# Kernel optimization log

Measured on AMD Instinct MI355X. Metric: run time of the kernel, lower is better.

## Reference

```python
import jax, jax.numpy as jnp
import numpy as np

B, C_IN, C_OUT, H, W = 4, 256, 256, 64, 64
K, STRIDE, PAD, DIL = 3, 1, 1, 1
KK = K * K


def setup_inputs() -> dict:
    key = jax.random.key(0)
    k1, k2, k3, k4 = jax.random.split(key, 4)
    x = jax.random.normal(k1, (B, C_IN, H, W), jnp.float32)
    # offset/mask conv weight (no bias), scaled small so offsets are modest
    w_mod = jax.random.normal(k2, (3 * KK, C_IN, K, K), jnp.float32) * 0.01
    # deform conv weight (xavier-ish scale) + bias
    w_def = jax.random.normal(k3, (C_OUT, C_IN, K, K), jnp.float32) * (1.0 / np.sqrt(C_IN * KK))
    b_def = jax.random.normal(k4, (C_OUT,), jnp.float32) * 0.01
    return {"x": x, "w_mod": w_mod, "w_def": w_def, "b_def": b_def}


def _conv_nchw(x, w, stride, pad):
    return jax.lax.conv_general_dilated(
        x, w, (stride, stride), [(pad, pad), (pad, pad)],
        dimension_numbers=("NCHW", "OIHW", "NCHW"))


def _bilinear_sample(x, py, px):
    # x: [B,C,H,W]; py/px: [B,KK,Ho,Wo] absolute sample coords (zero-pad outside)
    Bn, Cc, Hh, Ww = x.shape
    y0 = jnp.floor(py)
    x0 = jnp.floor(px)
    fy = py - y0
    fx = px - x0
    y0i = y0.astype(jnp.int32)
    x0i = x0.astype(jnp.int32)
    xf = x.reshape(Bn, Cc, Hh * Ww)

    def corner(yi, xi, wgt):
        valid = (yi >= 0) & (yi < Hh) & (xi >= 0) & (xi < Ww)
        yc = jnp.clip(yi, 0, Hh - 1)
        xc = jnp.clip(xi, 0, Ww - 1)
        idx = yc * Ww + xc                      # [B,KK,Ho,Wo]
        g = jax.vmap(lambda f, i: f[:, i])(xf, idx)  # [B,C,KK,Ho,Wo]
        return g * (wgt * valid)[:, None]

    return (corner(y0i, x0i, (1 - fy) * (1 - fx))
            + corner(y0i, x0i + 1, (1 - fy) * fx)
            + corner(y0i + 1, x0i, fy * (1 - fx))
            + corner(y0i + 1, x0i + 1, fy * fx))


def reference(x, w_mod, w_def, b_def):
    # offset/mask head
    mod = _conv_nchw(x, w_mod, STRIDE, PAD)          # [B, 3*KK, Ho, Wo]
    o1, o2, mask = mod[:, :KK], mod[:, KK:2 * KK], mod[:, 2 * KK:]
    offset = jnp.concatenate([o1, o2], axis=1)        # [B, 2*KK, Ho, Wo]
    # torchvision DeformConv2d: offset channels are interleaved (y, x) pairs
    dy = offset[:, 0::2]
    dx = offset[:, 1::2]
    mask = jax.nn.sigmoid(mask)                       # [B, KK, Ho, Wo]

    Ho, Wo = mod.shape[2], mod.shape[3]
    ky, kx = jnp.meshgrid(jnp.arange(K), jnp.arange(K), indexing="ij")
    ky = ky.reshape(-1).astype(jnp.float32)
    kx = kx.reshape(-1).astype(jnp.float32)
    base_y = (jnp.arange(Ho, dtype=jnp.float32) * STRIDE - PAD)[None, :, None] + (ky * DIL)[:, None, None]  # [KK,Ho,1]
    base_x = (jnp.arange(Wo, dtype=jnp.float32) * STRIDE - PAD)[None, None, :] + (kx * DIL)[:, None, None]  # [KK,1,Wo]
    py = dy + base_y[None]                            # [B,KK,Ho,Wo]
    px = dx + base_x[None]

    sampled = _bilinear_sample(x, py, px) * mask[:, None]  # [B,C,KK,Ho,Wo]
    out = jnp.einsum("bckhw,ock->bohw", sampled, w_def.reshape(C_OUT, C_IN, KK))
    return out + b_def[None, :, None, None]
```

## Files before the change

### kernel.cpp

```cpp
#include <hip/hip_runtime.h>

typedef unsigned short u16;
typedef unsigned int u32;
typedef short bf16x8 __attribute__((ext_vector_type(8)));
typedef float f32x4 __attribute__((ext_vector_type(4)));

#define CIN 256
#define COUT 256

__device__ __forceinline__ u16 f2b(float f) {
  u32 u = __float_as_uint(f);
  u += 0x7fffu + ((u >> 16) & 1u);
  return (u16)(u >> 16);
}
__device__ __forceinline__ u32 packbf(float lo, float hi) {
  return (u32)f2b(lo) | ((u32)f2b(hi) << 16);
}
__device__ __forceinline__ u32 bil2(u32 u00, u32 u01, u32 u10, u32 u11, float4 wt) {
  float s0 = __uint_as_float(u00 << 16) * wt.x;
  s0 = fmaf(__uint_as_float(u01 << 16), wt.y, s0);
  s0 = fmaf(__uint_as_float(u10 << 16), wt.z, s0);
  s0 = fmaf(__uint_as_float(u11 << 16), wt.w, s0);
  float s1 = __uint_as_float(u00 & 0xffff0000u) * wt.x;
  s1 = fmaf(__uint_as_float(u01 & 0xffff0000u), wt.y, s1);
  s1 = fmaf(__uint_as_float(u10 & 0xffff0000u), wt.z, s1);
  s1 = fmaf(__uint_as_float(u11 & 0xffff0000u), wt.w, s1);
  return packbf(s0, s1);
}
__device__ __forceinline__ void bar() {
  asm volatile("s_waitcnt lgkmcnt(0)\n\ts_barrier" ::: "memory");
}

__global__ __launch_bounds__(256) void k_prep(
    const float* __restrict__ x, const float* __restrict__ w_mod,
    const float* __restrict__ w_def,
    u16* __restrict__ xT, u16* __restrict__ Wm2, u16* __restrict__ W2) {
  __shared__ __align__(16) char SB[9216];
  int t = threadIdx.x, g = blockIdx.x;
  if (g < 1024) {
    u16 (*T)[72] = (u16(*)[72])SB;
    int b = g >> 8, ct = (g >> 6) & 3, pt = g & 63;
    int c0 = ct << 6, pos0 = pt << 6;
    {
      int cl = t >> 2, pb = (t & 3) << 4;
      const float* p = x + (((b << 8) + c0 + cl) << 12) + pos0 + pb;
#pragma unroll
      for (int i = 0; i < 4; ++i) {
        float4 v = *(const float4*)(p + i * 4);
        int pp = pb + i * 4;
        T[pp][cl] = f2b(v.x); T[pp + 1][cl] = f2b(v.y);
        T[pp + 2][cl] = f2b(v.z); T[pp + 3][cl] = f2b(v.w);
      }
    }
    __syncthreads();
    {
      int pl = t >> 2, q = t & 3;
      u16* dst = xT + (((b << 12) + pos0 + pl) << 8) + c0 + (q << 4);
      *(uint4*)dst = *(const uint4*)&T[pl][q << 4];
      *(uint4*)(dst + 8) = *(const uint4*)&T[pl][(q << 4) + 8];
    }
  } else {
    float* L = (float*)SB;
    int gg = g - 1024;
    if (gg < 256) {
      const float* src = w_def + gg * 2304;
      for (int j = t; j < 2304; j += 256) L[j] = src[j];
      __syncthreads();
      u16* dst = W2 + gg * 2304;
      for (int j = t; j < 2304; j += 256) {
        int kk = j >> 8, c = j & 255;
        dst[j] = f2b(L[c * 9 + kk]);
      }
    } else {
      int cm = gg - 256;
      if (cm < 27) {
        const float* src = w_mod + cm * 2304;
        for (int j = t; j < 2304; j += 256) L[j] = src[j];
      }
      __syncthreads();
      u16* dst = Wm2 + cm * 2304;
      for (int j = t; j < 2304; j += 256) {
        int kk = j >> 8, c = j & 255;
        dst[j] = (cm < 27) ? f2b(L[c * 9 + kk]) : (u16)0;
      }
    }
  }
}

__global__ __launch_bounds__(512) void k_fused(
    const u16* __restrict__ xT, const u16* __restrict__ Wm2,
    const u16* __restrict__ W2, const float* __restrict__ b_def,
    float* __restrict__ out) {
  __shared__ __align__(16) char LB[53760];
  __shared__ __align__(16) int2 Ci[576];
  __shared__ __align__(16) float4 Cw[576];
  u16 (*As1)[2][64][72] = (u16 (*)[2][64][72])LB;
  float (*mods2)[32][66] = (float (*)[32][66])(LB + 36864);
  u16 (*As2)[64][72] = (u16 (*)[64][72])LB;

  int t = threadIdx.x;
  int l = t & 63;
  int w = t >> 6;
  int h = t >> 8;
  int wl = w & 3;
  int tg = t & 255;
  int px = tg >> 2, q = tg & 3;
  int g = blockIdx.x;
  int b = (g & 7) >> 1, y = ((g >> 3) << 1) + (g & 1);
  const u16* xTb = xT + (b << 20);
  int ml = l & 15, kq = l >> 4;

  {
    f32x4 zero = {0.f, 0.f, 0.f, 0.f};
    f32x4 acc0 = zero, acc1 = zero;
    uint4 VA0, VA1, VB0, VB1;
    uint4 S0, S1, S2, S3, T0, T1, T2, T3;

#define MC_ISSUE_A(i, V0, V1)                                                \
  { int ch_ = h * 18 + (i); int kk_ = ch_ >> 2, c0_ = (ch_ & 3) << 6;        \
    int ky_ = kk_ / 3, kx_ = kk_ - 3 * ky_;                                  \
    int ys_ = y + ky_ - 1, xs_ = px + kx_ - 1;                               \
    V0 = make_uint4(0, 0, 0, 0); V1 = V0;                                    \
    if (ys_ >= 0 && ys_ < 64 && xs_ >= 0 && xs_ < 64) {                      \
      const u16* p_ = xTb + (((ys_ << 6) + xs_) << 8) + c0_ + (q << 4);      \
      V0 = *(const uint4*)p_; V1 = *(const uint4*)(p_ + 8);                  \
    } }

#define MC_ISSUE_B(i, R0, R1, R2, R3)                                        \
  { int ch_ = h * 18 + (i); int kk_ = ch_ >> 2, c0_ = (ch_ & 3) << 6;        \
    const u16* pw_ = Wm2 + (kk_ << 8) + c0_ + (kq << 3);                     \
    R0 = *(const uint4*)(pw_ + ml * 2304);                                   \
    R1 = *(const uint4*)(pw_ + (16 + ml) * 2304);                            \
    R2 = *(const uint4*)(pw_ + ml * 2304 + 32);                              \
    R3 = *(const uint4*)(pw_ + (16 + ml) * 2304 + 32); }

#define MC_WRITE(buf, V0, V1)                                                \
  { *(uint4*)&As1[h][buf][px][q << 4] = V0;                                  \
    *(uint4*)&As1[h][buf][px][(q << 4) + 8] = V1; }

#define MC_MFMA(buf, R0, R1, R2, R3)                                         \
  { bf16x8 a0_ = *(const bf16x8*)&As1[h][buf][wl * 16 + ml][kq << 3];        \
    acc0 = __builtin_amdgcn_mfma_f32_16x16x32_bf16(a0_, *(const bf16x8*)&R0, acc0, 0,0,0); \
    acc1 = __builtin_amdgcn_mfma_f32_16x16x32_bf16(a0_, *(const bf16x8*)&R1, acc1, 0,0,0); \
    bf16x8 a1_ = *(const bf16x8*)&As1[h][buf][wl * 16 + ml][32 + (kq << 3)]; \
    acc0 = __builtin_amdgcn_mfma_f32_16x16x32_bf16(a1_, *(const bf16x8*)&R2, acc0, 0,0,0); \
    acc1 = __builtin_amdgcn_mfma_f32_16x16x32_bf16(a1_, *(const bf16x8*)&R3, acc1, 0,0,0); }

    MC_ISSUE_A(0, VA0, VA1)
    MC_ISSUE_A(1, VB0, VB1)
    MC_ISSUE_B(0, S0, S1, S2, S3)
#pragma unroll 1
    for (int i2 = 0; i2 < 18; i2 += 2) {
      MC_WRITE(0, VA0, VA1)
      bar();
      if (i2 + 2 < 18) MC_ISSUE_A(i2 + 2, VA0, VA1)
      MC_ISSUE_B(i2 + 1, T0, T1, T2, T3)
      MC_MFMA(0, S0, S1, S2, S3)
      MC_WRITE(1, VB0, VB1)
      bar();
      if (i2 + 3 < 18) MC_ISSUE_A(i2 + 3, VB0, VB1)
      if (i2 + 2 < 18) MC_ISSUE_B(i2 + 2, S0, S1, S2, S3)
      MC_MFMA(1, T0, T1, T2, T3)
    }
#pragma unroll
    for (int r = 0; r < 4; ++r) {
      mods2[h][ml][wl * 16 + kq * 4 + r]      = acc0[r];
      mods2[h][16 + ml][wl * 16 + kq * 4 + r] = acc1[r];
    }
    __syncthreads();
    for (int i2 = t; i2 < 576; i2 += 512) {
      int kk = i2 >> 6, pxx_i = i2 & 63;
      float dy = mods2[0][2 * kk][pxx_i] + mods2[1][2 * kk][pxx_i];
      float dx = mods2[0][2 * kk + 1][pxx_i] + mods2[1][2 * kk + 1][pxx_i];
      float mv = mods2[0][18 + kk][pxx_i] + mods2[1][18 + kk][pxx_i];
      float msk = 1.f / (1.f + __expf(-mv));
      int ky = kk / 3, kx = kk - 3 * ky;
      float py  = dy + (float)(y + ky - 1);
      float pxx = dx + (float)(pxx_i + kx - 1);
      float y0f = floorf(py), x0f = floorf(pxx);
      float fy = py - y0f, fx = pxx - x0f;
      int y0 = (int)y0f, x0 = (int)x0f;
      float vy0 = (y0 >= 0 && y0 < 64) ? msk : 0.f;
      float vy1 = (y0 + 1 >= 0 && y0 + 1 < 64) ? msk : 0.f;
      float w00 = (1.f - fy) * (1.f - fx) * vy0;
      float w01 = (1.f - fy) * fx * vy0;
      float w10 = fy * (1.f - fx) * vy1;
      float w11 = fy * fx * vy1;
      int xb2 = min(max(x0, 0), 62);
      float wA0 = (xb2 == x0) ? w00 : ((xb2 == x0 + 1) ? w01 : 0.f);
      float wB0 = (xb2 + 1 == x0) ? w00 : ((xb2 + 1 == x0 + 1) ? w01 : 0.f);
      float wA1 = (xb2 == x0) ? w10 : ((xb2 == x0 + 1) ? w11 : 0.f);
      float wB1 = (xb2 + 1 == x0) ? w10 : ((xb2 + 1 == x0 + 1) ? w11 : 0.f);
      int ib0 = min(max(y0, 0), 63) * 64 + xb2;
      int ib1 = min(max(y0 + 1, 0), 63) * 64 + xb2;
      Ci[i2] = make_int2(ib0, ib1);
      Cw[i2] = make_float4(wA0, wB0, wA1, wB1);
    }
#undef MC_ISSUE_A
#undef MC_ISSUE_B
#undef MC_WRITE
#undef MC_MFMA
  }
  __syncthreads();

  {
    int gm = t >> 3, go = t & 7;
    int nrow0 = w * 32 + ml, nrow1 = nrow0 + 16;

    f32x4 zero = {0.f, 0.f, 0.f, 0.f};
    f32x4 acc[4][2];
#pragma unroll
    for (int i = 0; i < 4; ++i) { acc[i][0] = zero; acc[i][1] = zero; }

    uint4 A00, A01, A02, A03; float4 wt0;
    uint4 A10, A11, A12, A13; float4 wt1;
    uint4 RA0, RA1, RA2, RA3;
    uint4 RB0, RB1, RB2, RB3;

#define ISSUE_A(chunk, a0, a1, a2, a3, wt)                                   \
  { int kk_ = (chunk) >> 2, c0_ = ((chunk) & 3) << 6;                        \
    int cI_ = (kk_ << 6) + gm;                                               \
    int2 ib_ = Ci[cI_];                                                      \
    wt = Cw[cI_];                                                            \
    const u16* p0_ = xTb + (ib_.x << 8) + c0_ + (go << 3);                   \
    const u16* p1_ = xTb + (ib_.y << 8) + c0_ + (go << 3);                   \
    a0 = *(const uint4*)p0_;  a1 = *(const uint4*)(p0_ + 256);               \
    a2 = *(const uint4*)p1_;  a3 = *(const uint4*)(p1_ + 256); }

#define ISSUE_B(chunk, R0, R1, R2, R3)                                       \
  { int kk_ = (chunk) >> 2, c0_ = ((chunk) & 3) << 6;                        \
    const u16* pw_ = W2 + (kk_ << 8) + c0_ + (kq << 3);                      \
    R0 = *(const uint4*)(pw_ + nrow0 * 2304);                                \
    R1 = *(const uint4*)(pw_ + nrow1 * 2304);                                \
    R2 = *(const uint4*)(pw_ + nrow0 * 2304 + 32);                           \
    R3 = *(const uint4*)(pw_ + nrow1 * 2304 + 32); }

#define UNPACK(CUR, a0, a1, a2, a3, wt)                                      \
  { u32 q0_ = bil2(a0.x, a1.x, a2.x, a3.x, wt);                              \
    u32 q1_ = bil2(a0.y, a1.y, a2.y, a3.y, wt);                              \
    u32 q2_ = bil2(a0.z, a1.z, a2.z, a3.z, wt);                              \
    u32 q3_ = bil2(a0.w, a1.w, a2.w, a3.w, wt);                              \
    *(uint4*)&As2[CUR][gm][go << 3] = make_uint4(q0_, q1_, q2_, q3_); }

#define DOMFMA(CUR, R0, R1, R2, R3)                                          \
  { bf16x8 a0_ = *(const bf16x8*)&As2[CUR][ml][kq << 3];                     \
    bf16x8 a1_ = *(const bf16x8*)&As2[CUR][16 + ml][kq << 3];                \
    bf16x8 a2_ = *(const bf16x8*)&As2[CUR][32 + ml][kq << 3];                \
    bf16x8 a3_ = *(const bf16x8*)&As2[CUR][48 + ml][kq << 3];                \
    bf16x8 b0_ = *(const bf16x8*)&R0;                                        \
    bf16x8 b1_ = *(const bf16x8*)&R1;                                        \
    acc[0][0] = __builtin_amdgcn_mfma_f32_16x16x32_bf16(a0_, b0_, acc[0][0], 0,0,0); \
    acc[1][0] = __builtin_amdgcn_mfma_f32_16x16x32_bf16(a1_, b0_, acc[1][0], 0,0,0); \
    acc[2][0] = __builtin_amdgcn_mfma_f32_16x16x32_bf16(a2_, b0_, acc[2][0], 0,0,0); \
    acc[3][0] = __builtin_amdgcn_mfma_f32_16x16x32_bf16(a3_, b0_, acc[3][0], 0,0,0); \
    acc[0][1] = __builtin_amdgcn_mfma_f32_16x16x32_bf16(a0_, b1_, acc[0][1], 0,0,0); \
    acc[1][1] = __builtin_amdgcn_mfma_f32_16x16x32_bf16(a1_, b1_, acc[1][1], 0,0,0); \
    acc[2][1] = __builtin_amdgcn_mfma_f32_16x16x32_bf16(a2_, b1_, acc[2][1], 0,0,0); \
    acc[3][1] = __builtin_amdgcn_mfma_f32_16x16x32_bf16(a3_, b1_, acc[3][1], 0,0,0); \
    a0_ = *(const bf16x8*)&As2[CUR][ml][32 + (kq << 3)];                     \
    a1_ = *(const bf16x8*)&As2[CUR][16 + ml][32 + (kq << 3)];                \
    a2_ = *(const bf16x8*)&As2[CUR][32 + ml][32 + (kq << 3)];                \
    a3_ = *(const bf16x8*)&As2[CUR][48 + ml][32 + (kq << 3)];                \
    b0_ = *(const bf16x8*)&R2;                                               \
    b1_ = *(const bf16x8*)&R3;                                               \
    acc[0][0] = __builtin_amdgcn_mfma_f32_16x16x32_bf16(a0_, b0_, acc[0][0], 0,0,0); \
    acc[1][0] = __builtin_amdgcn_mfma_f32_16x16x32_bf16(a1_, b0_, acc[1][0], 0,0,0); \
    acc[2][0] = __builtin_amdgcn_mfma_f32_16x16x32_bf16(a2_, b0_, acc[2][0], 0,0,0); \
    acc[3][0] = __builtin_amdgcn_mfma_f32_16x16x32_bf16(a3_, b0_, acc[3][0], 0,0,0); \
    acc[0][1] = __builtin_amdgcn_mfma_f32_16x16x32_bf16(a0_, b1_, acc[0][1], 0,0,0); \
    acc[1][1] = __builtin_amdgcn_mfma_f32_16x16x32_bf16(a1_, b1_, acc[1][1], 0,0,0); \
    acc[2][1] = __builtin_amdgcn_mfma_f32_16x16x32_bf16(a2_, b1_, acc[2][1], 0,0,0); \
    acc[3][1] = __builtin_amdgcn_mfma_f32_16x16x32_bf16(a3_, b1_, acc[3][1], 0,0,0); }

    ISSUE_A(0, A00, A01, A02, A03, wt0)
    ISSUE_A(1, A10, A11, A12, A13, wt1)
    ISSUE_B(0, RA0, RA1, RA2, RA3)
#pragma unroll 1
    for (int c2 = 0; c2 < 36; c2 += 2) {
      UNPACK(0, A00, A01, A02, A03, wt0)
      bar();
      if (c2 + 2 < 36) ISSUE_A(c2 + 2, A00, A01, A02, A03, wt0)
      ISSUE_B(c2 + 1, RB0, RB1, RB2, RB3)
      DOMFMA(0, RA0, RA1, RA2, RA3)
      UNPACK(1, A10, A11, A12, A13, wt1)
      bar();
      if (c2 + 3 < 36) ISSUE_A(c2 + 3, A10, A11, A12, A13, wt1)
      if (c2 + 2 < 36) ISSUE_B(c2 + 2, RA0, RA1, RA2, RA3)
      DOMFMA(1, RB0, RB1, RB2, RB3)
    }

#pragma unroll
    for (int nt = 0; nt < 2; ++nt) {
      int n = w * 32 + nt * 16 + ml;
      float bias = b_def[n];
      float* op = out + (((b << 8) + n) << 12) + (y << 6);
#pragma unroll
      for (int mt = 0; mt < 4; ++mt) {
        float4 v;
        v.x = acc[mt][nt][0] + bias;
        v.y = acc[mt][nt][1] + bias;
        v.z = acc[mt][nt][2] + bias;
        v.w = acc[mt][nt][3] + bias;
        *(float4*)(op + mt * 16 + kq * 4) = v;
      }
    }
#undef ISSUE_A
#undef ISSUE_B
#undef UNPACK
#undef DOMFMA
  }
}

extern "C" void kernel_launch(void* const* d_in, const int* in_sizes, int n_in,
                              void* d_out, int out_size, void* d_ws, size_t ws_size,
                              hipStream_t stream) {
  const float* x     = (const float*)d_in[0];
  const float* w_mod = (const float*)d_in[1];
  const float* w_def = (const float*)d_in[2];
  const float* b_def = (const float*)d_in[3];
  float* out = (float*)d_out;
  char* ws = (char*)d_ws;
  u16* xT  = (u16*)(ws);
  u16* W2  = (u16*)(ws + 8388608);
  u16* Wm2 = (u16*)(ws + 8388608 + 1179648);

  hipLaunchKernelGGL(k_prep, dim3(1312), dim3(256), 0, stream, x, w_mod, w_def, xT, Wm2, W2);
  hipLaunchKernelGGL(k_fused, dim3(256), dim3(512), 0, stream, xT, Wm2, W2, b_def, out);
}
```

Before: 155.2 us.

## Process four K-chunks per barrier pair with deeper weight-register prefetch

Restructures the main MFMA loop so each iteration unpacks two gathered A chunks into shared memory, synchronises once, then runs MFMAs on both. Weight-fragment prefetch moves from two register sets to four (SA/SB/TA/TB), keeping B loads two chunks ahead. The aim is to halve the number of workgroup barriers per K chunk and give global loads more time to land before use. In exchange it raises register pressure, which may lower occupancy. It also needs four shared-memory A buffers, and that declaration does not appear in the change.

```diff
diff --git a/kernel.cpp b/kernel.cpp
--- a/kernel.cpp
+++ b/kernel.cpp
@@ -214,8 +214,10 @@
 
     uint4 A00, A01, A02, A03; float4 wt0;
     uint4 A10, A11, A12, A13; float4 wt1;
-    uint4 RA0, RA1, RA2, RA3;
-    uint4 RB0, RB1, RB2, RB3;
+    uint4 SA0, SA1, SA2, SA3;
+    uint4 SB0, SB1, SB2, SB3;
+    uint4 TA0, TA1, TA2, TA3;
+    uint4 TB0, TB1, TB2, TB3;
 
 #define ISSUE_A(chunk, a0, a1, a2, a3, wt)                                   \
   { int kk_ = (chunk) >> 2, c0_ = ((chunk) & 3) << 6;                        \
@@ -274,19 +276,31 @@
 
     ISSUE_A(0, A00, A01, A02, A03, wt0)
     ISSUE_A(1, A10, A11, A12, A13, wt1)
-    ISSUE_B(0, RA0, RA1, RA2, RA3)
+    ISSUE_B(0, SA0, SA1, SA2, SA3)
+    ISSUE_B(1, SB0, SB1, SB2, SB3)
 #pragma unroll 1
-    for (int c2 = 0; c2 < 36; c2 += 2) {
+    for (int p2 = 0; p2 < 9; ++p2) {
+      int c4 = p2 << 2;
       UNPACK(0, A00, A01, A02, A03, wt0)
-      bar();
-      if (c2 + 2 < 36) ISSUE_A(c2 + 2, A00, A01, A02, A03, wt0)
-      ISSUE_B(c2 + 1, RB0, RB1, RB2, RB3)
-      DOMFMA(0, RA0, RA1, RA2, RA3)
       UNPACK(1, A10, A11, A12, A13, wt1)
       bar();
-      if (c2 + 3 < 36) ISSUE_A(c2 + 3, A10, A11, A12, A13, wt1)
-      if (c2 + 2 < 36) ISSUE_B(c2 + 2, RA0, RA1, RA2, RA3)
-      DOMFMA(1, RB0, RB1, RB2, RB3)
+      ISSUE_A(c4 + 2, A00, A01, A02, A03, wt0)
+      ISSUE_A(c4 + 3, A10, A11, A12, A13, wt1)
+      ISSUE_B(c4 + 2, TA0, TA1, TA2, TA3)
+      ISSUE_B(c4 + 3, TB0, TB1, TB2, TB3)
+      DOMFMA(0, SA0, SA1, SA2, SA3)
+      DOMFMA(1, SB0, SB1, SB2, SB3)
+      UNPACK(2, A00, A01, A02, A03, wt0)
+      UNPACK(3, A10, A11, A12, A13, wt1)
+      bar();
+      if (p2 < 8) {
+        ISSUE_A(c4 + 4, A00, A01, A02, A03, wt0)
+        ISSUE_A(c4 + 5, A10, A11, A12, A13, wt1)
+        ISSUE_B(c4 + 4, SA0, SA1, SA2, SA3)
+        ISSUE_B(c4 + 5, SB0, SB1, SB2, SB3)
+      }
+      DOMFMA(2, TA0, TA1, TA2, TA3)
+      DOMFMA(3, TB0, TB1, TB2, TB3)
     }
 
 #pragma unroll
```

New measurement: 156.0 us. No clear change (+0.5%).

## Double block to 1024 threads and split deform GEMM across channel-chunk halves

Applied to the files above, without the earlier changes.

The fused kernel now launches 1024 threads per block. The offset/mask conv still runs on the first 512 threads while the others only match its barriers. The bilinear coefficient setup now uses one thread per entry. In the main deform GEMM each wave owns 16 output channels instead of 32, and the two block halves handle interleaved input-channel chunks through four LDS buffers. The aim is more resident waves per CU to hide gather and weight-load latency with a smaller per-thread accumulator, at the cost of tighter register budgets, idle threads in phase one and more barrier participants.

```diff
diff --git a/kernel.cpp b/kernel.cpp
--- a/kernel.cpp
+++ b/kernel.cpp
@@ -87,7 +87,7 @@
   }
 }
 
-__global__ __launch_bounds__(512) void k_fused(
+__global__ __launch_bounds__(1024) void k_fused(
     const u16* __restrict__ xT, const u16* __restrict__ Wm2,
     const u16* __restrict__ W2, const float* __restrict__ b_def,
     float* __restrict__ out) {
@@ -101,16 +101,16 @@
   int t = threadIdx.x;
   int l = t & 63;
   int w = t >> 6;
-  int h = t >> 8;
-  int wl = w & 3;
-  int tg = t & 255;
-  int px = tg >> 2, q = tg & 3;
   int g = blockIdx.x;
   int b = (g & 7) >> 1, y = ((g >> 3) << 1) + (g & 1);
   const u16* xTb = xT + (b << 20);
   int ml = l & 15, kq = l >> 4;
 
-  {
+  if (t < 512) {
+    int h = t >> 8;
+    int wl = (t >> 6) & 3;
+    int tg = t & 255;
+    int px = tg >> 2, q = tg & 3;
     f32x4 zero = {0.f, 0.f, 0.f, 0.f};
     f32x4 acc0 = zero, acc1 = zero;
     uint4 VA0, VA1, VB0, VB1;
@@ -167,55 +167,62 @@
       mods2[h][ml][wl * 16 + kq * 4 + r]      = acc0[r];
       mods2[h][16 + ml][wl * 16 + kq * 4 + r] = acc1[r];
     }
-    __syncthreads();
-    for (int i2 = t; i2 < 576; i2 += 512) {
-      int kk = i2 >> 6, pxx_i = i2 & 63;
-      float dy = mods2[0][2 * kk][pxx_i] + mods2[1][2 * kk][pxx_i];
-      float dx = mods2[0][2 * kk + 1][pxx_i] + mods2[1][2 * kk + 1][pxx_i];
-      float mv = mods2[0][18 + kk][pxx_i] + mods2[1][18 + kk][pxx_i];
-      float msk = 1.f / (1.f + __expf(-mv));
-      int ky = kk / 3, kx = kk - 3 * ky;
-      float py  = dy + (float)(y + ky - 1);
-      float pxx = dx + (float)(pxx_i + kx - 1);
-      float y0f = floorf(py), x0f = floorf(pxx);
-      float fy = py - y0f, fx = pxx - x0f;
-      int y0 = (int)y0f, x0 = (int)x0f;
-      float vy0 = (y0 >= 0 && y0 < 64) ? msk : 0.f;
-      float vy1 = (y0 + 1 >= 0 && y0 + 1 < 64) ? msk : 0.f;
-      float w00 = (1.f - fy) * (1.f - fx) * vy0;
-      float w01 = (1.f - fy) * fx * vy0;
-      float w10 = fy * (1.f - fx) * vy1;
-      float w11 = fy * fx * vy1;
-      int xb2 = min(max(x0, 0), 62);
-      float wA0 = (xb2 == x0) ? w00 : ((xb2 == x0 + 1) ? w01 : 0.f);
-      float wB0 = (xb2 + 1 == x0) ? w00 : ((xb2 + 1 == x0 + 1) ? w01 : 0.f);
-      float wA1 = (xb2 == x0) ? w10 : ((xb2 == x0 + 1) ? w11 : 0.f);
-      float wB1 = (xb2 + 1 == x0) ? w10 : ((xb2 + 1 == x0 + 1) ? w11 : 0.f);
-      int ib0 = min(max(y0, 0), 63) * 64 + xb2;
-      int ib1 = min(max(y0 + 1, 0), 63) * 64 + xb2;
-      Ci[i2] = make_int2(ib0, ib1);
-      Cw[i2] = make_float4(wA0, wB0, wA1, wB1);
-    }
 #undef MC_ISSUE_A
 #undef MC_ISSUE_B
 #undef MC_WRITE
 #undef MC_MFMA
+  } else {
+#pragma unroll 1
+    for (int i = 0; i < 9; ++i) { bar(); bar(); }
   }
   __syncthreads();
+  if (t < 576) {
+    int i2 = t;
+    int kk = i2 >> 6, pxx_i = i2 & 63;
+    float dy = mods2[0][2 * kk][pxx_i] + mods2[1][2 * kk][pxx_i];
+    float dx = mods2[0][2 * kk + 1][pxx_i] + mods2[1][2 * kk + 1][pxx_i];
+    float mv = mods2[0][18 + kk][pxx_i] + mods2[1][18 + kk][pxx_i];
+    float msk = 1.f / (1.f + __expf(-mv));
+    int ky = kk / 3, kx = kk - 3 * ky;
+    float py  = dy + (float)(y + ky - 1);
+    float pxx = dx + (float)(pxx_i + kx - 1);
+    float y0f = floorf(py), x0f = floorf(pxx);
+    float fy = py - y0f, fx = pxx - x0f;
+    int y0 = (int)y0f, x0 = (int)x0f;
+    float vy0 = (y0 >= 0 && y0 < 64) ? msk : 0.f;
+    float vy1 = (y0 + 1 >= 0 && y0 + 1 < 64) ? msk : 0.f;
+    float w00 = (1.f - fy) * (1.f - fx) * vy0;
+    float w01 = (1.f - fy) * fx * vy0;
+    float w10 = fy * (1.f - fx) * vy1;
+    float w11 = fy * fx * vy1;
+    int xb2 = min(max(x0, 0), 62);
+    float wA0 = (xb2 == x0) ? w00 : ((xb2 == x0 + 1) ? w01 : 0.f);
+    float wB0 = (xb2 + 1 == x0) ? w00 : ((xb2 + 1 == x0 + 1) ? w01 : 0.f);
+    float wA1 = (xb2 == x0) ? w10 : ((xb2 == x0 + 1) ? w11 : 0.f);
+    float wB1 = (xb2 + 1 == x0) ? w10 : ((xb2 + 1 == x0 + 1) ? w11 : 0.f);
+    int ib0 = min(max(y0, 0), 63) * 64 + xb2;
+    int ib1 = min(max(y0 + 1, 0), 63) * 64 + xb2;
+    Ci[i2] = make_int2(ib0, ib1);
+    Cw[i2] = make_float4(wA0, wB0, wA1, wB1);
+  }
+  __syncthreads();
 
   {
-    int gm = t >> 3, go = t & 7;
-    int nrow0 = w * 32 + ml, nrow1 = nrow0 + 16;
+    int cp = t >> 9;
+    int gm = (t >> 3) & 63, go = t & 7;
+    int nrow0 = (w << 4) + ml;
 
     f32x4 zero = {0.f, 0.f, 0.f, 0.f};
-    f32x4 acc[4][2];
+    f32x4 acc[4];
 #pragma unroll
-    for (int i = 0; i < 4; ++i) { acc[i][0] = zero; acc[i][1] = zero; }
+    for (int i = 0; i < 4; ++i) acc[i] = zero;
 
     uint4 A00, A01, A02, A03; float4 wt0;
     uint4 A10, A11, A12, A13; float4 wt1;
-    uint4 RA0, RA1, RA2, RA3;
-    uint4 RB0, RB1, RB2, RB3;
+    uint4 SA0, SA2;
+    uint4 SB0, SB2;
+    uint4 TA0, TA2;
+    uint4 TB0, TB2;
 
 #define ISSUE_A(chunk, a0, a1, a2, a3, wt)                                   \
   { int kk_ = (chunk) >> 2, c0_ = ((chunk) & 3) << 6;                        \
@@ -227,13 +234,11 @@
     a0 = *(const uint4*)p0_;  a1 = *(const uint4*)(p0_ + 256);               \
     a2 = *(const uint4*)p1_;  a3 = *(const uint4*)(p1_ + 256); }
 
-#define ISSUE_B(chunk, R0, R1, R2, R3)                                       \
+#define ISSUE_B(chunk, R0, R2)                                               \
   { int kk_ = (chunk) >> 2, c0_ = ((chunk) & 3) << 6;                        \
     const u16* pw_ = W2 + (kk_ << 8) + c0_ + (kq << 3);                      \
     R0 = *(const uint4*)(pw_ + nrow0 * 2304);                                \
-    R1 = *(const uint4*)(pw_ + nrow1 * 2304);                                \
-    R2 = *(const uint4*)(pw_ + nrow0 * 2304 + 32);                           \
-    R3 = *(const uint4*)(pw_ + nrow1 * 2304 + 32); }
+    R2 = *(const uint4*)(pw_ + nrow0 * 2304 + 32); }
 
 #define UNPACK(CUR, a0, a1, a2, a3, wt)                                      \
   { u32 q0_ = bil2(a0.x, a1.x, a2.x, a3.x, wt);                              \
@@ -242,65 +247,62 @@
     u32 q3_ = bil2(a0.w, a1.w, a2.w, a3.w, wt);                              \
     *(uint4*)&As2[CUR][gm][go << 3] = make_uint4(q0_, q1_, q2_, q3_); }
 
-#define DOMFMA(CUR, R0, R1, R2, R3)                                          \
+#define DOMFMA(CUR, R0, R2)                                                  \
   { bf16x8 a0_ = *(const bf16x8*)&As2[CUR][ml][kq << 3];                     \
     bf16x8 a1_ = *(const bf16x8*)&As2[CUR][16 + ml][kq << 3];                \
     bf16x8 a2_ = *(const bf16x8*)&As2[CUR][32 + ml][kq << 3];                \
     bf16x8 a3_ = *(const bf16x8*)&As2[CUR][48 + ml][kq << 3];                \
     bf16x8 b0_ = *(const bf16x8*)&R0;                                        \
-    bf16x8 b1_ = *(const bf16x8*)&R1;                                        \
-    acc[0][0] = __builtin_amdgcn_mfma_f32_16x16x32_bf16(a0_, b0_, acc[0][0], 0,0,0); \
-    acc[1][0] = __builtin_amdgcn_mfma_f32_16x16x32_bf16(a1_, b0_, acc[1][0], 0,0,0); \
-    acc[2][0] = __builtin_amdgcn_mfma_f32_16x16x32_bf16(a2_, b0_, acc[2][0], 0,0,0); \
-    acc[3][0] = __builtin_amdgcn_mfma_f32_16x16x32_bf16(a3_, b0_, acc[3][0], 0,0,0); \
-    acc[0][1] = __builtin_amdgcn_mfma_f32_16x16x32_bf16(a0_, b1_, acc[0][1], 0,0,0); \
-    acc[1][1] = __builtin_amdgcn_mfma_f32_16x16x32_bf16(a1_, b1_, acc[1][1], 0,0,0); \
-    acc[2][1] = __builtin_amdgcn_mfma_f32_16x16x32_bf16(a2_, b1_, acc[2][1], 0,0,0); \
-    acc[3][1] = __builtin_amdgcn_mfma_f32_16x16x32_bf16(a3_, b1_, acc[3][1], 0,0,0); \
+    acc[0] = __builtin_amdgcn_mfma_f32_16x16x32_bf16(a0_, b0_, acc[0], 0,0,0); \
+    acc[1] = __builtin_amdgcn_mfma_f32_16x16x32_bf16(a1_, b0_, acc[1], 0,0,0); \
+    acc[2] = __builtin_amdgcn_mfma_f32_16x16x32_bf16(a2_, b0_, acc[2], 0,0,0); \
+    acc[3] = __builtin_amdgcn_mfma_f32_16x16x32_bf16(a3_, b0_, acc[3], 0,0,0); \
     a0_ = *(const bf16x8*)&As2[CUR][ml][32 + (kq << 3)];                     \
     a1_ = *(const bf16x8*)&As2[CUR][16 + ml][32 + (kq << 3)];                \
     a2_ = *(const bf16x8*)&As2[CUR][32 + ml][32 + (kq << 3)];                \
     a3_ = *(const bf16x8*)&As2[CUR][48 + ml][32 + (kq << 3)];                \
     b0_ = *(const bf16x8*)&R2;                                               \
-    b1_ = *(const bf16x8*)&R3;                                               \
-    acc[0][0] = __builtin_amdgcn_mfma_f32_16x16x32_bf16(a0_, b0_, acc[0][0], 0,0,0); \
-    acc[1][0] = __builtin_amdgcn_mfma_f32_16x16x32_bf16(a1_, b0_, acc[1][0], 0,0,0); \
-    acc[2][0] = __builtin_amdgcn_mfma_f32_16x16x32_bf16(a2_, b0_, acc[2][0], 0,0,0); \
-    acc[3][0] = __builtin_amdgcn_mfma_f32_16x16x32_bf16(a3_, b0_, acc[3][0], 0,0,0); \
-    acc[0][1] = __builtin_amdgcn_mfma_f32_16x16x32_bf16(a0_, b1_, acc[0][1], 0,0,0); \
-    acc[1][1] = __builtin_amdgcn_mfma_f32_16x16x32_bf16(a1_, b1_, acc[1][1], 0,0,0); \
-    acc[2][1] = __builtin_amdgcn_mfma_f32_16x16x32_bf16(a2_, b1_, acc[2][1], 0,0,0); \
-    acc[3][1] = __builtin_amdgcn_mfma_f32_16x16x32_bf16(a3_, b1_, acc[3][1], 0,0,0); }
-
-    ISSUE_A(0, A00, A01, A02, A03, wt0)
-    ISSUE_A(1, A10, A11, A12, A13, wt1)
-    ISSUE_B(0, RA0, RA1, RA2, RA3)
+    acc[0] = __builtin_amdgcn_mfma_f32_16x16x32_bf16(a0_, b0_, acc[0], 0,0,0); \
+    acc[1] = __builtin_amdgcn_mfma_f32_16x16x32_bf16(a1_, b0_, acc[1], 0,0,0); \
+    acc[2] = __builtin_amdgcn_mfma_f32_16x16x32_bf16(a2_, b0_, acc[2], 0,0,0); \
+    acc[3] = __builtin_amdgcn_mfma_f32_16x16x32_bf16(a3_, b0_, acc[3], 0,0,0); }
+
+    ISSUE_A(0 + cp, A00, A01, A02, A03, wt0)
+    ISSUE_A(2 + cp, A10, A11, A12, A13, wt1)
+    ISSUE_B(0, SA0, SA2)
+    ISSUE_B(1, SB0, SB2)
 #pragma unroll 1
-    for (int c2 = 0; c2 < 36; c2 += 2) {
-      UNPACK(0, A00, A01, A02, A03, wt0)
+    for (int p2 = 0; p2 < 9; ++p2) {
+      int c4 = p2 << 2;
+      UNPACK(0 + cp, A00, A01, A02, A03, wt0)
       bar();
-      if (c2 + 2 < 36) ISSUE_A(c2 + 2, A00, A01, A02, A03, wt0)
-      ISSUE_B(c2 + 1, RB0, RB1, RB2, RB3)
-      DOMFMA(0, RA0, RA1, RA2, RA3)
-      UNPACK(1, A10, A11, A12, A13, wt1)
+      if (p2 < 8) ISSUE_A(c4 + 4 + cp, A00, A01, A02, A03, wt0)
+      ISSUE_B(c4 + 2, TA0, TA2)
+      ISSUE_B(c4 + 3, TB0, TB2)
+      DOMFMA(0, SA0, SA2)
+      DOMFMA(1, SB0, SB2)
+      UNPACK(2 + cp, A10, A11, A12, A13, wt1)
       bar();
-      if (c2 + 3 < 36) ISSUE_A(c2 + 3, A10, A11, A12, A13, wt1)
-      if (c2 + 2 < 36) ISSUE_B(c2 + 2, RA0, RA1, RA2, RA3)
-      DOMFMA(1, RB0, RB1, RB2, RB3)
-    }
-
-#pragma unroll
-    for (int nt = 0; nt < 2; ++nt) {
-      int n = w * 32 + nt * 16 + ml;
+      if (p2 < 8) {
+        ISSUE_A(c4 + 6 + cp, A10, A11, A12, A13, wt1)
+        ISSUE_B(c4 + 4, SA0, SA2)
+        ISSUE_B(c4 + 5, SB0, SB2)
+      }
+      DOMFMA(2, TA0, TA2)
+      DOMFMA(3, TB0, TB2)
+    }
+
+    {
+      int n = nrow0;
       float bias = b_def[n];
       float* op = out + (((b << 8) + n) << 12) + (y << 6);
 #pragma unroll
       for (int mt = 0; mt < 4; ++mt) {
         float4 v;
-        v.x = acc[mt][nt][0] + bias;
-        v.y = acc[mt][nt][1] + bias;
-        v.z = acc[mt][nt][2] + bias;
-        v.w = acc[mt][nt][3] + bias;
+        v.x = acc[mt][0] + bias;
+        v.y = acc[mt][1] + bias;
+        v.z = acc[mt][2] + bias;
+        v.w = acc[mt][3] + bias;
         *(float4*)(op + mt * 16 + kq * 4) = v;
       }
     }
@@ -325,5 +327,5 @@
   u16* Wm2 = (u16*)(ws + 8388608 + 1179648);
 
   hipLaunchKernelGGL(k_prep, dim3(1312), dim3(256), 0, stream, x, w_mod, w_def, xT, Wm2, W2);
-  hipLaunchKernelGGL(k_fused, dim3(256), dim3(512), 0, stream, xT, Wm2, W2, b_def, out);
-}
+  hipLaunchKernelGGL(k_fused, dim3(256), dim3(1024), 0, stream, xT, Wm2, W2, b_def, out);
+}
```

New measurement: 151.5 us. -2.4%, faster.
